# Optimization experiments

Hardware: AMD Instinct MI355X
Metric: run time of the kernel (lower is better)

The kernel has to match this reference:

```python
import jax, jax.numpy as jnp
import numpy as np

N_NODES = 100_000
N_EDGES = 800_000
D_IN = 64
HID = 32   # hidden_channels
OUT = 64   # out_channels
H1, H2, H3 = 7, 4, 1


def _lin(key, din, dout, scale=0.05):
    k1, k2 = jax.random.split(key)
    W = jax.random.normal(k1, (din, dout), jnp.float32) * scale
    b = jax.random.normal(k2, (dout,), jnp.float32) * scale
    return W, b


def setup_inputs() -> dict:
    key = jax.random.key(0)
    ks = jax.random.split(key, 16)
    x = jax.random.normal(ks[0], (N_NODES, D_IN), jnp.float32)
    edge_index = jax.random.randint(ks[1], (2, N_EDGES), 0, N_NODES, dtype=jnp.int32)
    inp = {"x": x, "edge_index": edge_index}
    # (in_dim, heads, per-head channels) for the 3 TransformerConv layers
    dims = [(D_IN, H1, HID), (H1 * HID, H2, HID), (H2 * HID, H3, OUT)]
    i = 2
    for l, (din, h, c) in enumerate(dims, start=1):
        for nm in ("q", "k", "v", "s"):  # query, key, value, skip linears
            W, b = _lin(ks[i], din, h * c)
            i += 1
            inp[f"W{nm}{l}"] = W
            inp[f"b{nm}{l}"] = b
    return inp


def _transformer_conv(x, src, dst, Wq, bq, Wk, bk, Wv, bv, Ws, bs, H, C):
    # PyG TransformerConv (concat=True, beta=False, root_weight=True, no edge feats)
    q = (x @ Wq + bq).reshape(-1, H, C)
    k = (x @ Wk + bk).reshape(-1, H, C)
    v = (x @ Wv + bv).reshape(-1, H, C)
    # per-edge attention logits [E, H]
    alpha = jnp.einsum('ehc,ehc->eh', q[dst], k[src]) / jnp.sqrt(jnp.asarray(C, q.dtype))
    # segment softmax over incoming edges of each dst node
    amax = jax.ops.segment_max(alpha, dst, num_segments=N_NODES)
    ex = jnp.exp(alpha - amax[dst])
    denom = jax.ops.segment_sum(ex, dst, num_segments=N_NODES)
    attn = ex / (denom[dst] + 1e-16)
    # weighted message aggregation [N, H, C] -> [N, H*C]
    msg = v[src] * attn[..., None]
    out = jax.ops.segment_sum(msg, dst, num_segments=N_NODES).reshape(N_NODES, H * C)
    # root/skip connection
    return out + x @ Ws + bs


def reference(x, edge_index,
              Wq1, bq1, Wk1, bk1, Wv1, bv1, Ws1, bs1,
              Wq2, bq2, Wk2, bk2, Wv2, bv2, Ws2, bs2,
              Wq3, bq3, Wk3, bk3, Wv3, bv3, Ws3, bs3):
    src, dst = edge_index[0], edge_index[1]
    h = jax.nn.relu(_transformer_conv(x, src, dst, Wq1, bq1, Wk1, bk1, Wv1, bv1, Ws1, bs1, H1, HID))
    h = jax.nn.relu(_transformer_conv(h, src, dst, Wq2, bq2, Wk2, bk2, Wv2, bv2, Ws2, bs2, H2, HID))
    return _transformer_conv(h, src, dst, Wq3, bq3, Wk3, bk3, Wv3, bv3, Ws3, bs3, H3, OUT)
```

## Files before the change

kernel.cpp:

```cpp
#include <hip/hip_runtime.h>
#include <hip/hip_bf16.h>
#include <math.h>

#define N_NODES 100000
#define N_EDGES 800000
#define SCAN_BLOCKS 98

typedef __attribute__((ext_vector_type(8))) short short8;
typedef __attribute__((ext_vector_type(4))) float f32x4;

__device__ __forceinline__ unsigned short f2b(float f) {
    __hip_bfloat16 h = __float2bfloat16(f);
    return *reinterpret_cast<unsigned short*>(&h);
}
__device__ __forceinline__ float2 up2(unsigned u) {
    unsigned lo = u << 16;
    unsigned hi = u & 0xffff0000u;
    float2 r;
    __builtin_memcpy(&r.x, &lo, 4);
    __builtin_memcpy(&r.y, &hi, 4);
    return r;
}


__global__ void hist_kernel(const int* __restrict__ dst, int* __restrict__ deg) {
    int e = blockIdx.x * blockDim.x + threadIdx.x;
    if (e < N_EDGES) atomicAdd(&deg[dst[e]], 1);
}

__global__ __launch_bounds__(1024) void scan_part(const int* __restrict__ deg,
                                                  int* __restrict__ rowptr,
                                                  int* __restrict__ partials) {
    __shared__ int buf[1024];
    const int t = threadIdx.x;
    const int i = blockIdx.x * 1024 + t;
    int x = (i < N_NODES) ? deg[i] : 0;
    buf[t] = x;
    __syncthreads();
    for (int off = 1; off < 1024; off <<= 1) {
        int y = (t >= off) ? buf[t - off] : 0;
        __syncthreads();
        buf[t] += y;
        __syncthreads();
    }
    if (i < N_NODES) rowptr[i] = buf[t] - x;
    if (t == 1023) partials[blockIdx.x] = buf[t];
}

__global__ __launch_bounds__(128) void scan_tail(int* __restrict__ partials,
                                                 int* __restrict__ rowptr) {
    __shared__ int buf[128];
    const int t = threadIdx.x;
    int x = (t < SCAN_BLOCKS) ? partials[t] : 0;
    buf[t] = x;
    __syncthreads();
    for (int off = 1; off < 128; off <<= 1) {
        int y = (t >= off) ? buf[t - off] : 0;
        __syncthreads();
        buf[t] += y;
        __syncthreads();
    }
    if (t < SCAN_BLOCKS) partials[t] = buf[t] - x;
    if (t == 127) rowptr[N_NODES] = buf[127];
}

__global__ __launch_bounds__(1024) void scan_add(int* __restrict__ rowptr,
                                                 const int* __restrict__ partials) {
    const int i = blockIdx.x * 1024 + threadIdx.x;
    if (i < N_NODES) rowptr[i] += partials[blockIdx.x];
}

__global__ void scatter_kernel(const int* __restrict__ src, const int* __restrict__ dst,
                               const int* __restrict__ rowptr, int* __restrict__ cursor,
                               int* __restrict__ sorted_src) {
    int e = blockIdx.x * blockDim.x + threadIdx.x;
    if (e < N_EDGES) {
        int d = dst[e];
        int pos = atomicAdd(&cursor[d], 1);
        sorted_src[rowptr[d] + pos] = src[e];
    }
}

__global__ void fill_kernel(float* __restrict__ out, int n, float val) {
    int i = blockIdx.x * blockDim.x + threadIdx.x;
    if (i < n) out[i] = val;
}


__global__ void convert_kernel(const float* __restrict__ X, unsigned short* __restrict__ Y, int n4) {
    int i = blockIdx.x * blockDim.x + threadIdx.x;
    if (i < n4) {
        float4 f = ((const float4*)X)[i];
        ushort4 u;
        u.x = f2b(f.x); u.y = f2b(f.y); u.z = f2b(f.z); u.w = f2b(f.w);
        ((ushort4*)Y)[i] = u;
    }
}

__global__ void build_wt(const float* __restrict__ Wq, const float* __restrict__ Wk,
                         const float* __restrict__ Wv, const float* __restrict__ Wsk,
                         const float* __restrict__ bq, const float* __restrict__ bk,
                         const float* __restrict__ bv, const float* __restrict__ bsk,
                         unsigned short* __restrict__ WT, float* __restrict__ biasF,
                         int K, int HC) {
    int total = 4 * HC * K;
    int idx = blockIdx.x * blockDim.x + threadIdx.x;
    if (idx >= total) return;
    int rowc = idx / K;
    int kk = idx - rowc * K;
    int sec = rowc / HC;
    int cw = rowc - sec * HC;
    const float* W = (sec == 0) ? Wq : (sec == 1) ? Wk : (sec == 2) ? Wv : Wsk;
    WT[idx] = f2b(W[(size_t)kk * HC + cw]);
    if (kk == 0) {
        const float* B = (sec == 0) ? bq : (sec == 1) ? bk : (sec == 2) ? bv : bsk;
        biasF[rowc] = B[cw];
    }
}


template <int K, bool YBF>
__global__ __launch_bounds__(256) void mfma_gemm(
    const unsigned short* __restrict__ Xb, const unsigned short* __restrict__ WT,
    const float* __restrict__ biasF, void* __restrict__ Y,
    int ncols, int ostride, int sec_size, int sec_stride, int h0C) {
    constexpr int STR = 40;
    constexpr int ESTR = 136;
    __shared__ __align__(16) char smem[128 * ESTR * 2];
    unsigned short* Xs = (unsigned short*)smem;
    unsigned short* Ws = (unsigned short*)(smem + 128 * STR * 2);
    const int t = threadIdx.x;
    const int wave = t >> 6, lane = t & 63, quad = lane >> 4, l16 = lane & 15;
    const int n0 = blockIdx.x * 128, c0 = blockIdx.y * 128;

    f32x4 acc[2][8];
#pragma unroll
    for (int i = 0; i < 2; ++i)
#pragma unroll
        for (int j = 0; j < 8; ++j)
#pragma unroll
            for (int r = 0; r < 4; ++r) acc[i][j][r] = 0.f;

    for (int k0 = 0; k0 < K; k0 += 32) {
#pragma unroll
        for (int i = 0; i < 2; ++i) {
            int idx = t + i * 256;
            int row = idx >> 2;
            int seg = (idx & 3) << 3;
            int gr = n0 + row;
            short8 xv;
#pragma unroll
            for (int z = 0; z < 8; ++z) xv[z] = 0;
            if (gr < N_NODES)
                xv = *(const short8*)(Xb + (size_t)gr * K + k0 + seg);
            *(short8*)(&Xs[row * STR + seg]) = xv;

            int c = c0 + row;
            short8 wv;
#pragma unroll
            for (int z = 0; z < 8; ++z) wv[z] = 0;
            if (c < ncols) {
                int sec = c / sec_size;
                int wtrow = sec * sec_stride + h0C + (c - sec * sec_size);
                wv = *(const short8*)(WT + (size_t)wtrow * K + k0 + seg);
            }
            *(short8*)(&Ws[row * STR + seg]) = wv;
        }
        __syncthreads();

        short8 af0 = *(short8*)(&Xs[(wave * 32 + l16) * STR + quad * 8]);
        short8 af1 = *(short8*)(&Xs[(wave * 32 + 16 + l16) * STR + quad * 8]);
#pragma unroll
        for (int ct = 0; ct < 8; ++ct) {
            short8 bfr = *(short8*)(&Ws[(ct * 16 + l16) * STR + quad * 8]);
            acc[0][ct] = __builtin_amdgcn_mfma_f32_16x16x32_bf16(af0, bfr, acc[0][ct], 0, 0, 0);
            acc[1][ct] = __builtin_amdgcn_mfma_f32_16x16x32_bf16(af1, bfr, acc[1][ct], 0, 0, 0);
        }
        __syncthreads();
    }

    if constexpr (YBF) {
        unsigned short* Es = (unsigned short*)smem;
#pragma unroll
        for (int ct = 0; ct < 8; ++ct) {
            if (c0 + ct * 16 >= ncols) break;
            int col = c0 + ct * 16 + l16;
            int sec = col / sec_size;
            float bv = biasF[sec * sec_stride + h0C + (col - sec * sec_size)];
#pragma unroll
            for (int rt = 0; rt < 2; ++rt)
#pragma unroll
                for (int r = 0; r < 4; ++r) {
                    int row = wave * 32 + rt * 16 + quad * 4 + r;
                    Es[row * ESTR + ct * 16 + l16] = f2b(acc[rt][ct][r] + bv);
                }
        }
        __syncthreads();
        const int erow = t >> 1;
        const int cb = (t & 1) * 8;
        const int gr = n0 + erow;
#pragma unroll
        for (int j = 0; j < 8; ++j) {
            int gc = c0 + j * 16 + cb;
            if (gr < N_NODES && gc < ncols)
                *(short8*)((unsigned short*)Y + (size_t)gr * ostride + gc) =
                    *(const short8*)(&Es[erow * ESTR + j * 16 + cb]);
        }
    } else {
#pragma unroll
        for (int ct = 0; ct < 8; ++ct) {
            int col = c0 + ct * 16 + l16;
            if (col >= ncols) continue;
            int sec = col / sec_size;
            float bv = biasF[sec * sec_stride + h0C + (col - sec * sec_size)];
#pragma unroll
            for (int rt = 0; rt < 2; ++rt) {
#pragma unroll
                for (int r = 0; r < 4; ++r) {
                    int row = n0 + wave * 32 + rt * 16 + quad * 4 + r;
                    if (row < N_NODES)
                        ((float*)Y)[(size_t)row * ostride + col] = acc[rt][ct][r] + bv;
                }
            }
        }
    }
}

template <int K, bool YBF>
static inline void launch_gemm(const unsigned short* Xb, const unsigned short* WT,
                               const float* biasF, void* Y, int ncols, int ostride,
                               int sec_size, int sec_stride, int h0C, hipStream_t s) {
    const int GX = (N_NODES + 127) / 128;
    int ny = (ncols + 127) / 128;
    mfma_gemm<K, YBF><<<dim3(GX, ny), 256, 0, s>>>(
        Xb, WT, biasF, Y, ncols, ostride, sec_size, sec_stride, h0C);
}


template <int C, int NH, bool RELU, bool YBF>
__global__ __launch_bounds__(256) void attn3(
    const unsigned short* __restrict__ F,
    const int* __restrict__ rowptr, const int* __restrict__ ssrc,
    void* __restrict__ Hv, int h0, int ostride) {
    constexpr int LPN = NH * C / 4;
    constexpr int NPW = 64 / LPN;
    constexpr int Ms = 3 * NH * C;
    constexpr int gC = NH * C;
    const int lane = threadIdx.x & 63;
    const int wave = (blockIdx.x * 256 + threadIdx.x) >> 6;
    const int slot = lane / LPN;
    const int cl = lane - slot * LPN;
    const int n = wave * NPW + slot;
    if (slot >= NPW || n >= N_NODES) return;

    const int head = cl / (C / 4);
    const int c4 = (cl - head * (C / 4)) * 4;
    const int qoff = head * C + c4;
    const float SCALE2 = ((C == 64) ? 0.125f : 0.17677669529663687f) * 1.44269504f;

    uint2 qu = *(const uint2*)(F + (size_t)n * Ms + qoff);
    float2 qa = up2(qu.x), qb = up2(qu.y);
    int s0 = rowptr[n], s1 = rowptr[n + 1];

    float l = 0.f, a0 = 0.f, a1 = 0.f, a2 = 0.f, a3 = 0.f;
    int ei = s0;
    for (; ei + 1 < s1; ei += 2) {
        int sA = ssrc[ei], sB = ssrc[ei + 1];
        const unsigned short* rA = F + (size_t)sA * Ms;
        const unsigned short* rB = F + (size_t)sB * Ms;
        uint2 kAu = *(const uint2*)(rA + gC + qoff);
        uint2 vAu = *(const uint2*)(rA + 2 * gC + qoff);
        uint2 kBu = *(const uint2*)(rB + gC + qoff);
        uint2 vBu = *(const uint2*)(rB + 2 * gC + qoff);
        float2 kA0 = up2(kAu.x), kA1 = up2(kAu.y);
        float2 kB0 = up2(kBu.x), kB1 = up2(kBu.y);
        float pA = fmaf(qa.x, kA0.x, qa.y * kA0.y) + fmaf(qb.x, kA1.x, qb.y * kA1.y);
        float pB = fmaf(qa.x, kB0.x, qa.y * kB0.y) + fmaf(qb.x, kB1.x, qb.y * kB1.y);
#pragma unroll
        for (int off = C / 8; off > 0; off >>= 1) {
            pA += __shfl_xor(pA, off);
            pB += __shfl_xor(pB, off);
        }
        float exA = exp2f(pA * SCALE2);
        float exB = exp2f(pB * SCALE2);
        float2 vA0 = up2(vAu.x), vA1 = up2(vAu.y);
        float2 vB0 = up2(vBu.x), vB1 = up2(vBu.y);
        l += exA + exB;
        a0 = fmaf(exA, vA0.x, fmaf(exB, vB0.x, a0));
        a1 = fmaf(exA, vA0.y, fmaf(exB, vB0.y, a1));
        a2 = fmaf(exA, vA1.x, fmaf(exB, vB1.x, a2));
        a3 = fmaf(exA, vA1.y, fmaf(exB, vB1.y, a3));
    }
    if (ei < s1) {
        int sA = ssrc[ei];
        const unsigned short* rA = F + (size_t)sA * Ms;
        uint2 kAu = *(const uint2*)(rA + gC + qoff);
        uint2 vAu = *(const uint2*)(rA + 2 * gC + qoff);
        float2 kA0 = up2(kAu.x), kA1 = up2(kAu.y);
        float pA = fmaf(qa.x, kA0.x, qa.y * kA0.y) + fmaf(qb.x, kA1.x, qb.y * kA1.y);
#pragma unroll
        for (int off = C / 8; off > 0; off >>= 1) pA += __shfl_xor(pA, off);
        float exA = exp2f(pA * SCALE2);
        float2 vA0 = up2(vAu.x), vA1 = up2(vAu.y);
        l += exA;
        a0 = fmaf(exA, vA0.x, a0);
        a1 = fmaf(exA, vA0.y, a1);
        a2 = fmaf(exA, vA1.x, a2);
        a3 = fmaf(exA, vA1.y, a3);
    }

    float inv = 1.f / (l + 1e-16f);
    float r0 = a0 * inv, r1 = a1 * inv, r2 = a2 * inv, r3 = a3 * inv;

    const int col = (h0 + head) * C + c4;
    if constexpr (YBF) {
        uint2* Hp = (uint2*)((unsigned short*)Hv + (size_t)n * ostride + col);
        uint2 hv = *Hp;
        float2 hx = up2(hv.x), hy = up2(hv.y);
        float o0 = hx.x + r0, o1 = hx.y + r1, o2 = hy.x + r2, o3 = hy.y + r3;
        if (RELU) {
            o0 = fmaxf(o0, 0.f); o1 = fmaxf(o1, 0.f);
            o2 = fmaxf(o2, 0.f); o3 = fmaxf(o3, 0.f);
        }
        uint2 pv;
        pv.x = (unsigned)f2b(o0) | ((unsigned)f2b(o1) << 16);
        pv.y = (unsigned)f2b(o2) | ((unsigned)f2b(o3) << 16);
        *Hp = pv;
    } else {
        float4* Hp = (float4*)((float*)Hv + (size_t)n * ostride + col);
        float4 h = *Hp;
        h.x += r0; h.y += r1; h.z += r2; h.w += r3;
        if (RELU) {
            h.x = fmaxf(h.x, 0.f); h.y = fmaxf(h.y, 0.f);
            h.z = fmaxf(h.z, 0.f); h.w = fmaxf(h.w, 0.f);
        }
        *Hp = h;
    }
}

static inline void launch_attn32(int NH, int h0, const unsigned short* F,
                                 void* H, int ostride, const int* rowptr,
                                 const int* ssrc, hipStream_t stream) {
    switch (NH) {
        case 1: attn3<32, 1, true, true><<<3125, 256, 0, stream>>>(F, rowptr, ssrc, H, h0, ostride); break;
        case 2: attn3<32, 2, true, true><<<6250, 256, 0, stream>>>(F, rowptr, ssrc, H, h0, ostride); break;
        case 3: attn3<32, 3, true, true><<<12500, 256, 0, stream>>>(F, rowptr, ssrc, H, h0, ostride); break;
        case 4: attn3<32, 4, true, true><<<12500, 256, 0, stream>>>(F, rowptr, ssrc, H, h0, ostride); break;
        default: attn3<32, 7, true, true><<<25000, 256, 0, stream>>>(F, rowptr, ssrc, H, h0, ostride); break;
    }
}


extern "C" void kernel_launch(void* const* d_in, const int* in_sizes, int n_in,
                              void* d_out, int out_size, void* d_ws, size_t ws_size,
                              hipStream_t stream) {
    const float* x = (const float*)d_in[0];
    const int* ei = (const int*)d_in[1];
    const int* srcp = ei;
    const int* dstp = ei + N_EDGES;

    const float* W[12];
    const float* B[12];
    for (int i = 0; i < 12; ++i) {
        W[i] = (const float*)d_in[2 + 2 * i];
        B[i] = (const float*)d_in[3 + 2 * i];
    }
    float* out = (float*)d_out;

    char* p = (char*)d_ws;
    size_t off = 0;
    unsigned short* wt  = (unsigned short*)(p + off); off += 240000;
    float* biasF        = (float*)(p + off);          off += 4096;
    int* rowptr = (int*)(p + off); off += sizeof(int) * (N_NODES + 1);
    int* deg    = (int*)(p + off); off += sizeof(int) * N_NODES;
    int* cursor = (int*)(p + off); off += sizeof(int) * N_NODES;
    int* partials = (int*)(p + off); off += sizeof(int) * 128;
    int* ssrc   = (int*)(p + off); off += sizeof(int) * N_EDGES;
    off = (off + 255) & ~(size_t)255;
    unsigned short* h1  = (unsigned short*)(p + off); off += (size_t)224 * N_NODES * 2;
    unsigned short* h2  = (unsigned short*)(p + off); off += (size_t)128 * N_NODES * 2;
    unsigned short* xb1 = (unsigned short*)(p + off); off += (size_t)64 * N_NODES * 2;
    unsigned short* tail = (unsigned short*)(p + off);

    if (ws_size < off + 6500000) {
        fill_kernel<<<(out_size + 255) / 256, 256, 0, stream>>>(out, out_size, (float)(ws_size >> 20));
        return;
    }
    size_t tail_bytes = ws_size - off;
    const size_t F1PASS = (size_t)3 * 32 * N_NODES * 2;

    int nh1[7], np1 = 0;
    int nh2[4], np2 = 0;
    unsigned short *F1w, *F2w;
    if (tail_bytes >= 7 * F1PASS) {
        nh1[np1++] = 7;
        nh2[np2++] = 4;
        F1w = F2w = tail;
    } else if (tail_bytes >= 4 * F1PASS) {
        nh1[np1++] = 4; nh1[np1++] = 3;
        nh2[np2++] = 4;
        F1w = F2w = tail;
    } else if (tail_bytes >= 2 * F1PASS) {
        nh1[np1++] = 2; nh1[np1++] = 2; nh1[np1++] = 2; nh1[np1++] = 1;
        nh2[np2++] = 2; nh2[np2++] = 2;
        F1w = F2w = tail;
    } else {
        for (int i = 0; i < 7; ++i) nh1[np1++] = 1;
        for (int i = 0; i < 4; ++i) nh2[np2++] = 1;
        F1w = h2;
        F2w = xb1;
    }
    unsigned short* F3 = h1;

    hipMemsetAsync(deg, 0, sizeof(int) * 2 * N_NODES, stream);
    hist_kernel<<<(N_EDGES + 255) / 256, 256, 0, stream>>>(dstp, deg);
    scan_part<<<SCAN_BLOCKS, 1024, 0, stream>>>(deg, rowptr, partials);
    scan_tail<<<1, 128, 0, stream>>>(partials, rowptr);
    scan_add<<<SCAN_BLOCKS, 1024, 0, stream>>>(rowptr, partials);
    scatter_kernel<<<(N_EDGES + 255) / 256, 256, 0, stream>>>(srcp, dstp, rowptr, cursor, ssrc);

    convert_kernel<<<(N_NODES * 64 / 4 + 255) / 256, 256, 0, stream>>>(x, xb1, N_NODES * 64 / 4);

    build_wt<<<(4 * 224 * 64 + 255) / 256, 256, 0, stream>>>(
        W[0], W[1], W[2], W[3], B[0], B[1], B[2], B[3], wt, biasF, 64, 224);
    launch_gemm<64, true>(xb1, wt + (size_t)3 * 224 * 64, biasF + 3 * 224, h1,
                          224, 224, 224, 0, 0, stream);
    {
        int h0 = 0;
        for (int pass = 0; pass < np1; ++pass) {
            int NH = nh1[pass];
            int nc = 3 * NH * 32;
            launch_gemm<64, true>(xb1, wt, biasF, F1w, nc, nc, NH * 32, 224, h0 * 32, stream);
            launch_attn32(NH, h0, F1w, h1, 224, rowptr, ssrc, stream);
            h0 += NH;
        }
    }

    build_wt<<<(4 * 128 * 224 + 255) / 256, 256, 0, stream>>>(
        W[4], W[5], W[6], W[7], B[4], B[5], B[6], B[7], wt, biasF, 224, 128);
    launch_gemm<224, true>(h1, wt + (size_t)3 * 128 * 224, biasF + 3 * 128, h2,
                           128, 128, 128, 0, 0, stream);
    {
        int h0 = 0;
        for (int pass = 0; pass < np2; ++pass) {
            int NH = nh2[pass];
            int nc = 3 * NH * 32;
            launch_gemm<224, true>(h1, wt, biasF, F2w, nc, nc, NH * 32, 128, h0 * 32, stream);
            launch_attn32(NH, h0, F2w, h2, 128, rowptr, ssrc, stream);
            h0 += NH;
        }
    }

    build_wt<<<(4 * 64 * 128 + 255) / 256, 256, 0, stream>>>(
        W[8], W[9], W[10], W[11], B[8], B[9], B[10], B[11], wt, biasF, 128, 64);
    launch_gemm<128, true>(h2, wt, biasF, F3, 192, 192, 64, 64, 0, stream);
    launch_gemm<128, false>(h2, wt + (size_t)3 * 64 * 128, biasF + 3 * 64, out,
                            64, 64, 64, 0, 0, stream);
    attn3<64, 1, false, false><<<6250, 256, 0, stream>>>(F3, rowptr, ssrc, out, 0, 64);
}
```

Before: 676.1 us.

## Interleave K and V columns per lane and unroll edge gather by four

The weight-building kernel now lays out the K and V projection columns interleaved in groups of four per head, so that each lane's key and value slices are adjacent in the fused QKV buffer. The attention kernel then fetches both with a single 16-byte load per edge rather than two 8-byte loads. The edge loop is unrolled from two to four for more memory-level parallelism, and the softmax scale is folded into q once. The GEMM section mapping is simplified to a split/offset scheme. More registers are live per thread in exchange.

```diff
diff --git a/kernel.cpp b/kernel.cpp
--- a/kernel.cpp
+++ b/kernel.cpp
@@ -20,6 +20,14 @@
     __builtin_memcpy(&r.x, &lo, 4);
     __builtin_memcpy(&r.y, &hi, 4);
     return r;
+}
+__device__ __forceinline__ float dot4(float2 qa, float2 qb, unsigned k0, unsigned k1) {
+    float2 x = up2(k0), y = up2(k1);
+    float p = x.x * qa.x;
+    p = fmaf(x.y, qa.y, p);
+    p = fmaf(y.x, qb.x, p);
+    p = fmaf(y.y, qb.y, p);
+    return p;
 }
 
 
@@ -102,20 +110,29 @@
                          const float* __restrict__ bq, const float* __restrict__ bk,
                          const float* __restrict__ bv, const float* __restrict__ bsk,
                          unsigned short* __restrict__ WT, float* __restrict__ biasF,
-                         int K, int HC) {
+                         int K, int HC, int C) {
     int total = 4 * HC * K;
     int idx = blockIdx.x * blockDim.x + threadIdx.x;
     if (idx >= total) return;
     int rowc = idx / K;
     int kk = idx - rowc * K;
-    int sec = rowc / HC;
-    int cw = rowc - sec * HC;
-    const float* W = (sec == 0) ? Wq : (sec == 1) ? Wk : (sec == 2) ? Wv : Wsk;
+    const float* W;
+    const float* Bp;
+    int cw;
+    if (rowc < HC) {
+        W = Wq; Bp = bq; cw = rowc;
+    } else if (rowc < 3 * HC) {
+        int u = rowc - HC;
+        int h = u / (2 * C);
+        int rr = u - h * 2 * C;
+        int grp = rr >> 3, w = rr & 7;
+        if (w < 4) { W = Wk;  Bp = bk;  cw = h * C + grp * 4 + w; }
+        else       { W = Wv;  Bp = bv;  cw = h * C + grp * 4 + w - 4; }
+    } else {
+        W = Wsk; Bp = bsk; cw = rowc - 3 * HC;
+    }
     WT[idx] = f2b(W[(size_t)kk * HC + cw]);
-    if (kk == 0) {
-        const float* B = (sec == 0) ? bq : (sec == 1) ? bk : (sec == 2) ? bv : bsk;
-        biasF[rowc] = B[cw];
-    }
+    if (kk == 0) biasF[rowc] = Bp[cw];
 }
 
 
@@ -123,7 +140,7 @@
 __global__ __launch_bounds__(256) void mfma_gemm(
     const unsigned short* __restrict__ Xb, const unsigned short* __restrict__ WT,
     const float* __restrict__ biasF, void* __restrict__ Y,
-    int ncols, int ostride, int sec_size, int sec_stride, int h0C) {
+    int ncols, int ostride, int split, int rq, int rkv) {
     constexpr int STR = 40;
     constexpr int ESTR = 136;
     __shared__ __align__(16) char smem[128 * ESTR * 2];
@@ -160,8 +177,7 @@
 #pragma unroll
             for (int z = 0; z < 8; ++z) wv[z] = 0;
             if (c < ncols) {
-                int sec = c / sec_size;
-                int wtrow = sec * sec_stride + h0C + (c - sec * sec_size);
+                int wtrow = (c < split) ? (rq + c) : (rkv + (c - split));
                 wv = *(const short8*)(WT + (size_t)wtrow * K + k0 + seg);
             }
             *(short8*)(&Ws[row * STR + seg]) = wv;
@@ -185,8 +201,8 @@
         for (int ct = 0; ct < 8; ++ct) {
             if (c0 + ct * 16 >= ncols) break;
             int col = c0 + ct * 16 + l16;
-            int sec = col / sec_size;
-            float bv = biasF[sec * sec_stride + h0C + (col - sec * sec_size)];
+            int brow = (col < split) ? (rq + col) : (rkv + (col - split));
+            float bv = biasF[brow];
 #pragma unroll
             for (int rt = 0; rt < 2; ++rt)
 #pragma unroll
@@ -211,8 +227,8 @@
         for (int ct = 0; ct < 8; ++ct) {
             int col = c0 + ct * 16 + l16;
             if (col >= ncols) continue;
-            int sec = col / sec_size;
-            float bv = biasF[sec * sec_stride + h0C + (col - sec * sec_size)];
+            int brow = (col < split) ? (rq + col) : (rkv + (col - split));
+            float bv = biasF[brow];
 #pragma unroll
             for (int rt = 0; rt < 2; ++rt) {
 #pragma unroll
@@ -229,11 +245,11 @@
 template <int K, bool YBF>
 static inline void launch_gemm(const unsigned short* Xb, const unsigned short* WT,
                                const float* biasF, void* Y, int ncols, int ostride,
-                               int sec_size, int sec_stride, int h0C, hipStream_t s) {
+                               int split, int rq, int rkv, hipStream_t s) {
     const int GX = (N_NODES + 127) / 128;
     int ny = (ncols + 127) / 128;
     mfma_gemm<K, YBF><<<dim3(GX, ny), 256, 0, s>>>(
-        Xb, WT, biasF, Y, ncols, ostride, sec_size, sec_stride, h0C);
+        Xb, WT, biasF, Y, ncols, ostride, split, rq, rkv);
 }
 
 
@@ -244,8 +260,8 @@
     void* __restrict__ Hv, int h0, int ostride) {
     constexpr int LPN = NH * C / 4;
     constexpr int NPW = 64 / LPN;
-    constexpr int Ms = 3 * NH * C;
     constexpr int gC = NH * C;
+    constexpr int Ms = 3 * gC;
     const int lane = threadIdx.x & 63;
     const int wave = (blockIdx.x * 256 + threadIdx.x) >> 6;
     const int slot = lane / LPN;
@@ -256,57 +272,78 @@
     const int head = cl / (C / 4);
     const int c4 = (cl - head * (C / 4)) * 4;
     const int qoff = head * C + c4;
+    const int kvoff = gC + head * 2 * C + 2 * c4;
     const float SCALE2 = ((C == 64) ? 0.125f : 0.17677669529663687f) * 1.44269504f;
 
     uint2 qu = *(const uint2*)(F + (size_t)n * Ms + qoff);
     float2 qa = up2(qu.x), qb = up2(qu.y);
+    qa.x *= SCALE2; qa.y *= SCALE2; qb.x *= SCALE2; qb.y *= SCALE2;
     int s0 = rowptr[n], s1 = rowptr[n + 1];
 
     float l = 0.f, a0 = 0.f, a1 = 0.f, a2 = 0.f, a3 = 0.f;
     int ei = s0;
-    for (; ei + 1 < s1; ei += 2) {
-        int sA = ssrc[ei], sB = ssrc[ei + 1];
-        const unsigned short* rA = F + (size_t)sA * Ms;
-        const unsigned short* rB = F + (size_t)sB * Ms;
-        uint2 kAu = *(const uint2*)(rA + gC + qoff);
-        uint2 vAu = *(const uint2*)(rA + 2 * gC + qoff);
-        uint2 kBu = *(const uint2*)(rB + gC + qoff);
-        uint2 vBu = *(const uint2*)(rB + 2 * gC + qoff);
-        float2 kA0 = up2(kAu.x), kA1 = up2(kAu.y);
-        float2 kB0 = up2(kBu.x), kB1 = up2(kBu.y);
-        float pA = fmaf(qa.x, kA0.x, qa.y * kA0.y) + fmaf(qb.x, kA1.x, qb.y * kA1.y);
-        float pB = fmaf(qa.x, kB0.x, qa.y * kB0.y) + fmaf(qb.x, kB1.x, qb.y * kB1.y);
+    for (; ei + 3 < s1; ei += 4) {
+        int iA = ssrc[ei], iB = ssrc[ei + 1], iC = ssrc[ei + 2], iD = ssrc[ei + 3];
+        uint4 A = *(const uint4*)(F + (size_t)iA * Ms + kvoff);
+        uint4 B = *(const uint4*)(F + (size_t)iB * Ms + kvoff);
+        uint4 Cv = *(const uint4*)(F + (size_t)iC * Ms + kvoff);
+        uint4 D = *(const uint4*)(F + (size_t)iD * Ms + kvoff);
+        float pA = dot4(qa, qb, A.x, A.y);
+        float pB = dot4(qa, qb, B.x, B.y);
+        float pC = dot4(qa, qb, Cv.x, Cv.y);
+        float pD = dot4(qa, qb, D.x, D.y);
 #pragma unroll
         for (int off = C / 8; off > 0; off >>= 1) {
             pA += __shfl_xor(pA, off);
             pB += __shfl_xor(pB, off);
-        }
-        float exA = exp2f(pA * SCALE2);
-        float exB = exp2f(pB * SCALE2);
-        float2 vA0 = up2(vAu.x), vA1 = up2(vAu.y);
-        float2 vB0 = up2(vBu.x), vB1 = up2(vBu.y);
-        l += exA + exB;
-        a0 = fmaf(exA, vA0.x, fmaf(exB, vB0.x, a0));
-        a1 = fmaf(exA, vA0.y, fmaf(exB, vB0.y, a1));
-        a2 = fmaf(exA, vA1.x, fmaf(exB, vB1.x, a2));
-        a3 = fmaf(exA, vA1.y, fmaf(exB, vB1.y, a3));
+            pC += __shfl_xor(pC, off);
+            pD += __shfl_xor(pD, off);
+        }
+        float eA = exp2f(pA), eB = exp2f(pB), eC = exp2f(pC), eD = exp2f(pD);
+        l += (eA + eB) + (eC + eD);
+        float2 vA0 = up2(A.z), vA1 = up2(A.w);
+        float2 vB0 = up2(B.z), vB1 = up2(B.w);
+        float2 vC0 = up2(Cv.z), vC1 = up2(Cv.w);
+        float2 vD0 = up2(D.z), vD1 = up2(D.w);
+        a0 = fmaf(eA, vA0.x, fmaf(eB, vB0.x, fmaf(eC, vC0.x, fmaf(eD, vD0.x, a0))));
+        a1 = fmaf(eA, vA0.y, fmaf(eB, vB0.y, fmaf(eC, vC0.y, fmaf(eD, vD0.y, a1))));
+        a2 = fmaf(eA, vA1.x, fmaf(eB, vB1.x, fmaf(eC, vC1.x, fmaf(eD, vD1.x, a2))));
+        a3 = fmaf(eA, vA1.y, fmaf(eB, vB1.y, fmaf(eC, vC1.y, fmaf(eD, vD1.y, a3))));
+    }
+    if (ei + 1 < s1) {
+        int iA = ssrc[ei], iB = ssrc[ei + 1];
+        ei += 2;
+        uint4 A = *(const uint4*)(F + (size_t)iA * Ms + kvoff);
+        uint4 B = *(const uint4*)(F + (size_t)iB * Ms + kvoff);
+        float pA = dot4(qa, qb, A.x, A.y);
+        float pB = dot4(qa, qb, B.x, B.y);
+#pragma unroll
+        for (int off = C / 8; off > 0; off >>= 1) {
+            pA += __shfl_xor(pA, off);
+            pB += __shfl_xor(pB, off);
+        }
+        float eA = exp2f(pA), eB = exp2f(pB);
+        l += eA + eB;
+        float2 vA0 = up2(A.z), vA1 = up2(A.w);
+        float2 vB0 = up2(B.z), vB1 = up2(B.w);
+        a0 = fmaf(eA, vA0.x, fmaf(eB, vB0.x, a0));
+        a1 = fmaf(eA, vA0.y, fmaf(eB, vB0.y, a1));
+        a2 = fmaf(eA, vA1.x, fmaf(eB, vB1.x, a2));
+        a3 = fmaf(eA, vA1.y, fmaf(eB, vB1.y, a3));
     }
     if (ei < s1) {
-        int sA = ssrc[ei];
-        const unsigned short* rA = F + (size_t)sA * Ms;
-        uint2 kAu = *(const uint2*)(rA + gC + qoff);
-        uint2 vAu = *(const uint2*)(rA + 2 * gC + qoff);
-        float2 kA0 = up2(kAu.x), kA1 = up2(kAu.y);
-        float pA = fmaf(qa.x, kA0.x, qa.y * kA0.y) + fmaf(qb.x, kA1.x, qb.y * kA1.y);
+        int iA = ssrc[ei];
+        uint4 A = *(const uint4*)(F + (size_t)iA * Ms + kvoff);
+        float pA = dot4(qa, qb, A.x, A.y);
 #pragma unroll
         for (int off = C / 8; off > 0; off >>= 1) pA += __shfl_xor(pA, off);
-        float exA = exp2f(pA * SCALE2);
-        float2 vA0 = up2(vAu.x), vA1 = up2(vAu.y);
-        l += exA;
-        a0 = fmaf(exA, vA0.x, a0);
-        a1 = fmaf(exA, vA0.y, a1);
-        a2 = fmaf(exA, vA1.x, a2);
-        a3 = fmaf(exA, vA1.y, a3);
+        float eA = exp2f(pA);
+        l += eA;
+        float2 vA0 = up2(A.z), vA1 = up2(A.w);
+        a0 = fmaf(eA, vA0.x, a0);
+        a1 = fmaf(eA, vA0.y, a1);
+        a2 = fmaf(eA, vA1.x, a2);
+        a3 = fmaf(eA, vA1.y, a3);
     }
 
     float inv = 1.f / (l + 1e-16f);
@@ -422,7 +459,7 @@
     convert_kernel<<<(N_NODES * 64 / 4 + 255) / 256, 256, 0, stream>>>(x, xb1, N_NODES * 64 / 4);
 
     build_wt<<<(4 * 224 * 64 + 255) / 256, 256, 0, stream>>>(
-        W[0], W[1], W[2], W[3], B[0], B[1], B[2], B[3], wt, biasF, 64, 224);
+        W[0], W[1], W[2], W[3], B[0], B[1], B[2], B[3], wt, biasF, 64, 224, 32);
     launch_gemm<64, true>(xb1, wt + (size_t)3 * 224 * 64, biasF + 3 * 224, h1,
                           224, 224, 224, 0, 0, stream);
     {
@@ -430,14 +467,16 @@
         for (int pass = 0; pass < np1; ++pass) {
             int NH = nh1[pass];
             int nc = 3 * NH * 32;
-            launch_gemm<64, true>(xb1, wt, biasF, F1w, nc, nc, NH * 32, 224, h0 * 32, stream);
+            launch_gemm<64, true>(xb1, wt, biasF, F1w, nc, nc,
+                                  NH * 32, h0 * 32,
+                                  224 + 2 * h0 * 32, stream);
             launch_attn32(NH, h0, F1w, h1, 224, rowptr, ssrc, stream);
             h0 += NH;
         }
     }
 
     build_wt<<<(4 * 128 * 224 + 255) / 256, 256, 0, stream>>>(
-        W[4], W[5], W[6], W[7], B[4], B[5], B[6], B[7], wt, biasF, 224, 128);
+        W[4], W[5], W[6], W[7], B[4], B[5], B[6], B[7], wt, biasF, 224, 128, 32);
     launch_gemm<224, true>(h1, wt + (size_t)3 * 128 * 224, biasF + 3 * 128, h2,
                            128, 128, 128, 0, 0, stream);
     {
@@ -445,15 +484,18 @@
         for (int pass = 0; pass < np2; ++pass) {
             int NH = nh2[pass];
             int nc = 3 * NH * 32;
-            launch_gemm<224, true>(h1, wt, biasF, F2w, nc, nc, NH * 32, 128, h0 * 32, stream);
+            launch_gemm<224, true>(h1, wt, biasF, F2w, nc, nc,
+                                   NH * 32, h0 * 32,
+                                   128 + 2 * h0 * 32, stream);
             launch_attn32(NH, h0, F2w, h2, 128, rowptr, ssrc, stream);
             h0 += NH;
         }
     }
 
     build_wt<<<(4 * 64 * 128 + 255) / 256, 256, 0, stream>>>(
-        W[8], W[9], W[10], W[11], B[8], B[9], B[10], B[11], wt, biasF, 128, 64);
-    launch_gemm<128, true>(h2, wt, biasF, F3, 192, 192, 64, 64, 0, stream);
+        W[8], W[9], W[10], W[11], B[8], B[9], B[10], B[11], wt, biasF, 128, 64, 64);
+    launch_gemm<128, true>(h2, wt, biasF, F3, 192, 192,
+                           64, 0, 64, stream);
     launch_gemm<128, false>(h2, wt + (size_t)3 * 64 * 128, biasF + 3 * 64, out,
                             64, 64, 64, 0, 0, stream);
     attn3<64, 1, false, false><<<6250, 256, 0, stream>>>(F3, rowptr, ssrc, out, 0, 64);
```

New measurement: 665.5 us. No clear change (-1.6%).
